# Kernel tuning notes

Measured on AMD Instinct MI355X. Metric: run time of the kernel, lower is better.

Reference implementation:

```python
import jax, jax.numpy as jnp
import numpy as np

D = 640
I = 640
K = 4  # experts per token
E = 32
T = 64
EPS = 1e-5
LIMIT = 7.0


def setup_inputs() -> dict:
    key = jax.random.key(0)
    ks = jax.random.split(key, 8)
    return {
        "x": jax.random.normal(ks[0], (1, D, 1, T), dtype=jnp.float32),
        "norm_w": jax.random.uniform(ks[1], (D,), dtype=jnp.float32) + 0.5,
        "gate_w": jax.random.normal(ks[2], (E, D), dtype=jnp.float32) * 0.05,
        "gate_b": jax.random.normal(ks[3], (E,), dtype=jnp.float32) * 0.05,
        "w1": jax.random.normal(ks[4], (E, D, 2 * I), dtype=jnp.float32) * 0.02,
        "b1": jax.random.normal(ks[5], (E, 2 * I), dtype=jnp.float32) * 0.02,
        "w2": jax.random.normal(ks[6], (E, I, D), dtype=jnp.float32) * 0.02,
        "b2": jax.random.normal(ks[7], (E, D), dtype=jnp.float32) * 0.02,
    }


def reference(x, norm_w, gate_w, gate_b, w1, b1, w2, b2):
    residual = x
    # RMSNorm over channel dim (axis=1) of (1, D, 1, T)
    var = jnp.mean(x * x, axis=1, keepdims=True)
    normed = x * jax.lax.rsqrt(var + EPS) * norm_w.reshape(-1, 1, 1)
    # (1, D, 1, T) -> (T, D)
    t = normed[0, :, 0, :].T
    # router
    g = t @ gate_w.T + gate_b                       # (T, E)
    top_vals, top_idx = jax.lax.top_k(g, K)        # (T, K)
    ew = jax.nn.softmax(top_vals, axis=-1)          # (T, K)
    # gather per-token expert weights (faithful to index_select pattern)
    w1s = w1[top_idx]                               # (T, K, D, 2I)
    b1s = b1[top_idx]                               # (T, K, 2I)
    h = jnp.einsum('td,tkdi->tki', t, w1s) + b1s    # (T, K, 2I)
    h_glu = jnp.minimum(h[..., :I], LIMIT)
    h_lin = jnp.clip(h[..., I:], -LIMIT, LIMIT)
    h_act = h_glu * jax.nn.sigmoid(1.702 * h_glu) * (h_lin + 1.0)  # (T, K, I)
    out = jnp.einsum('tki,tkid->tkd', h_act, w2[top_idx]) + b2[top_idx]  # (T, K, D)
    out = jnp.sum(out * ew[..., None], axis=1)      # (T, D)
    out = out.T[None, :, None, :]                   # (1, D, 1, T)
    return residual + out
```

## Files before the change

### kernel.cpp

```cpp
#include <hip/hip_runtime.h>
#include <math.h>

#define DDIM 640
#define IDIM 640
#define TWO_I 1280
#define KSEL 4
#define NEXP 32
#define NTOK 64
#define NPAIR 256
#define EPSV 1e-5f
#define LIMIT 7.0f
#define CHUNK 8
#define RC 8
#define RLEN 80


__global__ void k_rmsnorm(const float* __restrict__ x, const float* __restrict__ nw,
                          float* __restrict__ tws, int* __restrict__ counts) {
    const int t = blockIdx.x;
    const int tid = threadIdx.x;
    if (blockIdx.x == 0 && tid < NEXP) counts[tid] = 0;
    __shared__ float red[256];
    float s = 0.f;
    for (int d = tid; d < DDIM; d += 256) {
        float v = x[d * NTOK + t];
        s += v * v;
    }
    red[tid] = s;
    __syncthreads();
    for (int off = 128; off > 0; off >>= 1) {
        if (tid < off) red[tid] += red[tid + off];
        __syncthreads();
    }
    const float rs = 1.0f / sqrtf(red[0] * (1.0f / DDIM) + EPSV);
    for (int d = tid; d < DDIM; d += 256) {
        tws[t * DDIM + d] = x[d * NTOK + t] * rs * nw[d];
    }
}

__global__ void k_router(const float* __restrict__ tws, const float* __restrict__ gw,
                         const float* __restrict__ gb, float* __restrict__ ew,
                         int* __restrict__ counts, int* __restrict__ list,
                         int* __restrict__ pexp) {
    const int t = blockIdx.x;
    const int lane = threadIdx.x;
    __shared__ float lg[NEXP];
    if (lane < NEXP) {
        const float* g = gw + lane * DDIM;
        const float* tr = tws + t * DDIM;
        float acc = 0.f;
        for (int d = 0; d < DDIM; d += 4) {
            acc = fmaf(tr[d], g[d], acc);
            acc = fmaf(tr[d + 1], g[d + 1], acc);
            acc = fmaf(tr[d + 2], g[d + 2], acc);
            acc = fmaf(tr[d + 3], g[d + 3], acc);
        }
        lg[lane] = acc + gb[lane];
    }
    __syncthreads();
    if (lane == 0) {
        float vals[KSEL];
        int idx[KSEL];
        for (int k = 0; k < KSEL; ++k) {
            float best = -1e30f;
            int bi = 0;
            for (int e = 0; e < NEXP; ++e) {
                float v = lg[e];
                if (v > best) { best = v; bi = e; }
            }
            vals[k] = best;
            idx[k] = bi;
            lg[bi] = -1e30f;
        }
        const float m = vals[0];
        float ex[KSEL];
        float se = 0.f;
        for (int k = 0; k < KSEL; ++k) { ex[k] = __expf(vals[k] - m); se += ex[k]; }
        const float inv = 1.0f / se;
        for (int k = 0; k < KSEL; ++k) {
            const int p = t * KSEL + k;
            ew[p] = ex[k] * inv;
            pexp[p] = idx[k];
            const int slot = atomicAdd(&counts[idx[k]], 1);
            list[idx[k] * NTOK + slot] = p;
        }
    }
}

__global__ __launch_bounds__(64) void k_ffn1(const float* __restrict__ tws,
                                             const float* __restrict__ w1,
                                             float* __restrict__ hpart,
                                             const int* __restrict__ counts,
                                             const int* __restrict__ list) {
    const int e = blockIdx.y;
    const int rc = blockIdx.z >> 3;
    const int tc = blockIdx.z & 7;
    const int cnt = counts[e];
    const int c0 = tc * CHUNK;
    if (c0 >= cnt) return;
    const int col0 = blockIdx.x * 256 + threadIdx.x * 4;
    const int d0 = rc * RLEN;

    __shared__ float tl[CHUNK][RLEN];
    int pid[CHUNK];
#pragma unroll
    for (int s = 0; s < CHUNK; ++s) {
        int ii = c0 + s;
        ii = (ii < cnt) ? ii : c0;
        pid[s] = list[e * NTOK + ii];
    }
    for (int s = 0; s < CHUNK; ++s) {
        const int tok = pid[s] >> 2;
        for (int d = threadIdx.x; d < RLEN; d += 64)
            tl[s][d] = tws[tok * DDIM + d0 + d];
    }
    __syncthreads();

    const float* wp = w1 + (size_t)e * DDIM * TWO_I + (size_t)d0 * TWO_I + col0;
    float acc[CHUNK][4];
#pragma unroll
    for (int s = 0; s < CHUNK; ++s)
#pragma unroll
        for (int c = 0; c < 4; ++c) acc[s][c] = 0.f;

    for (int dd = 0; dd < RLEN; dd += 8) {
        float4 w[8];
#pragma unroll
        for (int u = 0; u < 8; ++u)
            w[u] = *reinterpret_cast<const float4*>(wp + (size_t)(dd + u) * TWO_I);
#pragma unroll
        for (int u = 0; u < 8; ++u) {
#pragma unroll
            for (int s = 0; s < CHUNK; ++s) {
                const float tv = tl[s][dd + u];
                acc[s][0] = fmaf(tv, w[u].x, acc[s][0]);
                acc[s][1] = fmaf(tv, w[u].y, acc[s][1]);
                acc[s][2] = fmaf(tv, w[u].z, acc[s][2]);
                acc[s][3] = fmaf(tv, w[u].w, acc[s][3]);
            }
        }
    }

#pragma unroll
    for (int s = 0; s < CHUNK; ++s) {
        float4 v = make_float4(acc[s][0], acc[s][1], acc[s][2], acc[s][3]);
        *reinterpret_cast<float4*>(&hpart[((size_t)rc * NPAIR + pid[s]) * TWO_I + col0]) = v;
    }
}

__global__ void k_reduce1(const float* __restrict__ hpart, const float* __restrict__ b1,
                          const int* __restrict__ pexp, float* __restrict__ hact) {
    const int p = blockIdx.x;
    const int e = pexp[p];
    for (int i = threadIdx.x; i < IDIM; i += 256) {
        float g = 0.f, l = 0.f;
#pragma unroll
        for (int rc = 0; rc < RC; ++rc) {
            g += hpart[((size_t)rc * NPAIR + p) * TWO_I + i];
            l += hpart[((size_t)rc * NPAIR + p) * TWO_I + i + IDIM];
        }
        float hg = fminf(g + b1[e * TWO_I + i], LIMIT);
        float hl = l + b1[e * TWO_I + IDIM + i];
        hl = fminf(fmaxf(hl, -LIMIT), LIMIT);
        const float sig = 1.0f / (1.0f + __expf(-1.702f * hg));
        hact[(size_t)p * IDIM + i] = hg * sig * (hl + 1.0f);
    }
}

__global__ __launch_bounds__(64) void k_ffn2(const float* __restrict__ hact,
                                             const float* __restrict__ w2,
                                             float* __restrict__ hpart2,
                                             const int* __restrict__ counts,
                                             const int* __restrict__ list) {
    const int e = blockIdx.y;
    const int rc = blockIdx.z >> 3;
    const int tc = blockIdx.z & 7;
    const int cnt = counts[e];
    const int c0 = tc * CHUNK;
    if (c0 >= cnt) return;
    const int col0 = blockIdx.x * 128 + threadIdx.x * 2;
    const int i0 = rc * RLEN;

    __shared__ float hl[CHUNK][RLEN];
    int pid[CHUNK];
#pragma unroll
    for (int s = 0; s < CHUNK; ++s) {
        int ii = c0 + s;
        ii = (ii < cnt) ? ii : c0;
        pid[s] = list[e * NTOK + ii];
    }
    for (int s = 0; s < CHUNK; ++s) {
        for (int i = threadIdx.x; i < RLEN; i += 64)
            hl[s][i] = hact[(size_t)pid[s] * IDIM + i0 + i];
    }
    __syncthreads();

    const float* wp = w2 + (size_t)e * IDIM * DDIM + (size_t)i0 * DDIM + col0;
    float acc[CHUNK][2];
#pragma unroll
    for (int s = 0; s < CHUNK; ++s) {
        acc[s][0] = 0.f;
        acc[s][1] = 0.f;
    }

    for (int ii = 0; ii < RLEN; ii += 8) {
        float2 w[8];
#pragma unroll
        for (int u = 0; u < 8; ++u)
            w[u] = *reinterpret_cast<const float2*>(wp + (size_t)(ii + u) * DDIM);
#pragma unroll
        for (int u = 0; u < 8; ++u) {
#pragma unroll
            for (int s = 0; s < CHUNK; ++s) {
                const float hv = hl[s][ii + u];
                acc[s][0] = fmaf(hv, w[u].x, acc[s][0]);
                acc[s][1] = fmaf(hv, w[u].y, acc[s][1]);
            }
        }
    }

#pragma unroll
    for (int s = 0; s < CHUNK; ++s) {
        float2 v = make_float2(acc[s][0], acc[s][1]);
        *reinterpret_cast<float2*>(&hpart2[((size_t)rc * NPAIR + pid[s]) * DDIM + col0]) = v;
    }
}

__global__ void k_final(const float* __restrict__ x, const float* __restrict__ hpart2,
                        const float* __restrict__ b2, const float* __restrict__ ew,
                        const int* __restrict__ pexp, float* __restrict__ out) {
    const int t = blockIdx.x;
    for (int d = threadIdx.x; d < DDIM; d += 256) {
        float v = x[d * NTOK + t];
#pragma unroll
        for (int k = 0; k < KSEL; ++k) {
            const int p = t * KSEL + k;
            const int e = pexp[p];
            float s = 0.f;
#pragma unroll
            for (int rc = 0; rc < RC; ++rc)
                s += hpart2[((size_t)rc * NPAIR + p) * DDIM + d];
            v += (s + b2[e * DDIM + d]) * ew[p];
        }
        out[d * NTOK + t] = v;
    }
}

extern "C" void kernel_launch(void* const* d_in, const int* in_sizes, int n_in,
                              void* d_out, int out_size, void* d_ws, size_t ws_size,
                              hipStream_t stream) {
    const float* x  = (const float*)d_in[0];
    const float* nw = (const float*)d_in[1];
    const float* gw = (const float*)d_in[2];
    const float* gb = (const float*)d_in[3];
    const float* w1 = (const float*)d_in[4];
    const float* b1 = (const float*)d_in[5];
    const float* w2 = (const float*)d_in[6];
    const float* b2 = (const float*)d_in[7];
    float* out = (float*)d_out;

    float* ws    = (float*)d_ws;
    float* tws   = ws;
    float* hact  = ws + 40960;
    float* hpart = ws + 204800;
    float* ew    = ws + 2826240;
    int* counts  = (int*)(ws + 2826496);
    int* list    = (int*)(ws + 2826528);
    int* pexp    = (int*)(ws + 2828576);

    hipLaunchKernelGGL(k_rmsnorm, dim3(NTOK), dim3(256), 0, stream, x, nw, tws, counts);
    hipLaunchKernelGGL(k_router, dim3(NTOK), dim3(64), 0, stream, tws, gw, gb, ew, counts, list, pexp);
    hipLaunchKernelGGL(k_ffn1, dim3(5, NEXP, RC * 8), dim3(64), 0, stream, tws, w1, hpart, counts, list);
    hipLaunchKernelGGL(k_reduce1, dim3(NPAIR), dim3(256), 0, stream, hpart, b1, pexp, hact);
    hipLaunchKernelGGL(k_ffn2, dim3(5, NEXP, RC * 8), dim3(64), 0, stream, hact, w2, hpart, counts, list);
    hipLaunchKernelGGL(k_final, dim3(NTOK), dim3(256), 0, stream, x, hpart, b2, ew, pexp, out);
}
```

Baseline: 80.70 us.

## Restructure MoE FFN grids: wider blocks, smaller token chunks, XCD-aware block mapping

Both expert GEMM kernels now run one 320-thread block that covers the full output width instead of five 64-thread blocks. Token chunks shrink from 8 to 4, with 16 chunk slots per expert. The reduction dimension is split into 16 pieces when the workspace is large enough, and a flat block index is remapped so consecutive logical blocks spread across the 8 XCDs. The aim is more parallelism and better load balance for a small, skewed token count. The costs are that each weight row is re-read by more token chunks, and the larger split increases partial-sum traffic through the reduce and final kernels.

```diff
diff --git a/kernel.cpp b/kernel.cpp
--- a/kernel.cpp
+++ b/kernel.cpp
@@ -10,9 +10,9 @@
 #define NPAIR 256
 #define EPSV 1e-5f
 #define LIMIT 7.0f
-#define CHUNK 8
-#define RC 8
-#define RLEN 80
+#define CHUNK 4
+#define NTC 16
+#define MAXRLEN 80
 
 
 __global__ void k_rmsnorm(const float* __restrict__ x, const float* __restrict__ nw,
@@ -87,21 +87,30 @@
     }
 }
 
-__global__ __launch_bounds__(64) void k_ffn1(const float* __restrict__ tws,
-                                             const float* __restrict__ w1,
-                                             float* __restrict__ hpart,
-                                             const int* __restrict__ counts,
-                                             const int* __restrict__ list) {
-    const int e = blockIdx.y;
-    const int rc = blockIdx.z >> 3;
-    const int tc = blockIdx.z & 7;
+__global__ __launch_bounds__(320) void k_ffn1(const float* __restrict__ tws,
+                                              const float* __restrict__ w1,
+                                              float* __restrict__ hpart,
+                                              const int* __restrict__ counts,
+                                              const int* __restrict__ list,
+                                              int nrcMask, int eShift, int rlen) {
+    const int cpx = (int)gridDim.x >> 3;
+    const int L = (blockIdx.x & 7) * cpx + (blockIdx.x >> 3);
+    const int tc = L & (NTC - 1);
+    const int tmp = L >> 4;
+    const int rc = tmp & nrcMask;
+    const int e = tmp >> eShift;
+
     const int cnt = counts[e];
     const int c0 = tc * CHUNK;
     if (c0 >= cnt) return;
-    const int col0 = blockIdx.x * 256 + threadIdx.x * 4;
-    const int d0 = rc * RLEN;
-
-    __shared__ float tl[CHUNK][RLEN];
+    const int tid = threadIdx.x;
+    const int wid = tid >> 6;
+    const int lane = tid & 63;
+    const int col0 = wid * 256 + lane * 4;
+    const int d0 = rc * rlen;
+
+    __shared__ float tl[CHUNK][MAXRLEN];
+
     int pid[CHUNK];
 #pragma unroll
     for (int s = 0; s < CHUNK; ++s) {
@@ -109,30 +118,30 @@
         ii = (ii < cnt) ? ii : c0;
         pid[s] = list[e * NTOK + ii];
     }
-    for (int s = 0; s < CHUNK; ++s) {
-        const int tok = pid[s] >> 2;
-        for (int d = threadIdx.x; d < RLEN; d += 64)
-            tl[s][d] = tws[tok * DDIM + d0 + d];
-    }
+#pragma unroll
+    for (int s = 0; s < CHUNK; ++s)
+        for (int d = tid; d < rlen; d += 320)
+            tl[s][d] = tws[(pid[s] >> 2) * DDIM + d0 + d];
     __syncthreads();
 
     const float* wp = w1 + (size_t)e * DDIM * TWO_I + (size_t)d0 * TWO_I + col0;
+
     float acc[CHUNK][4];
 #pragma unroll
     for (int s = 0; s < CHUNK; ++s)
 #pragma unroll
         for (int c = 0; c < 4; ++c) acc[s][c] = 0.f;
 
-    for (int dd = 0; dd < RLEN; dd += 8) {
+    for (int rb = 0; rb < rlen; rb += 8) {
         float4 w[8];
 #pragma unroll
         for (int u = 0; u < 8; ++u)
-            w[u] = *reinterpret_cast<const float4*>(wp + (size_t)(dd + u) * TWO_I);
+            w[u] = *reinterpret_cast<const float4*>(wp + (size_t)(rb + u) * TWO_I);
 #pragma unroll
         for (int u = 0; u < 8; ++u) {
 #pragma unroll
             for (int s = 0; s < CHUNK; ++s) {
-                const float tv = tl[s][dd + u];
+                const float tv = tl[s][rb + u];
                 acc[s][0] = fmaf(tv, w[u].x, acc[s][0]);
                 acc[s][1] = fmaf(tv, w[u].y, acc[s][1]);
                 acc[s][2] = fmaf(tv, w[u].z, acc[s][2]);
@@ -149,13 +158,12 @@
 }
 
 __global__ void k_reduce1(const float* __restrict__ hpart, const float* __restrict__ b1,
-                          const int* __restrict__ pexp, float* __restrict__ hact) {
+                          const int* __restrict__ pexp, float* __restrict__ hact, int nrc) {
     const int p = blockIdx.x;
     const int e = pexp[p];
     for (int i = threadIdx.x; i < IDIM; i += 256) {
         float g = 0.f, l = 0.f;
-#pragma unroll
-        for (int rc = 0; rc < RC; ++rc) {
+        for (int rc = 0; rc < nrc; ++rc) {
             g += hpart[((size_t)rc * NPAIR + p) * TWO_I + i];
             l += hpart[((size_t)rc * NPAIR + p) * TWO_I + i + IDIM];
         }
@@ -167,21 +175,28 @@
     }
 }
 
-__global__ __launch_bounds__(64) void k_ffn2(const float* __restrict__ hact,
-                                             const float* __restrict__ w2,
-                                             float* __restrict__ hpart2,
-                                             const int* __restrict__ counts,
-                                             const int* __restrict__ list) {
-    const int e = blockIdx.y;
-    const int rc = blockIdx.z >> 3;
-    const int tc = blockIdx.z & 7;
+__global__ __launch_bounds__(320) void k_ffn2(const float* __restrict__ hact,
+                                              const float* __restrict__ w2,
+                                              float* __restrict__ hpart2,
+                                              const int* __restrict__ counts,
+                                              const int* __restrict__ list,
+                                              int nrcMask, int eShift, int rlen) {
+    const int cpx = (int)gridDim.x >> 3;
+    const int L = (blockIdx.x & 7) * cpx + (blockIdx.x >> 3);
+    const int tc = L & (NTC - 1);
+    const int tmp = L >> 4;
+    const int rc = tmp & nrcMask;
+    const int e = tmp >> eShift;
+
     const int cnt = counts[e];
     const int c0 = tc * CHUNK;
     if (c0 >= cnt) return;
-    const int col0 = blockIdx.x * 128 + threadIdx.x * 2;
-    const int i0 = rc * RLEN;
-
-    __shared__ float hl[CHUNK][RLEN];
+    const int tid = threadIdx.x;
+    const int col0 = tid * 2;
+    const int i0 = rc * rlen;
+
+    __shared__ float tl[CHUNK][MAXRLEN];
+
     int pid[CHUNK];
 #pragma unroll
     for (int s = 0; s < CHUNK; ++s) {
@@ -189,30 +204,28 @@
         ii = (ii < cnt) ? ii : c0;
         pid[s] = list[e * NTOK + ii];
     }
-    for (int s = 0; s < CHUNK; ++s) {
-        for (int i = threadIdx.x; i < RLEN; i += 64)
-            hl[s][i] = hact[(size_t)pid[s] * IDIM + i0 + i];
-    }
+#pragma unroll
+    for (int s = 0; s < CHUNK; ++s)
+        for (int d = tid; d < rlen; d += 320)
+            tl[s][d] = hact[(size_t)pid[s] * IDIM + i0 + d];
     __syncthreads();
 
     const float* wp = w2 + (size_t)e * IDIM * DDIM + (size_t)i0 * DDIM + col0;
+
     float acc[CHUNK][2];
 #pragma unroll
-    for (int s = 0; s < CHUNK; ++s) {
-        acc[s][0] = 0.f;
-        acc[s][1] = 0.f;
-    }
-
-    for (int ii = 0; ii < RLEN; ii += 8) {
+    for (int s = 0; s < CHUNK; ++s) { acc[s][0] = 0.f; acc[s][1] = 0.f; }
+
+    for (int rb = 0; rb < rlen; rb += 8) {
         float2 w[8];
 #pragma unroll
         for (int u = 0; u < 8; ++u)
-            w[u] = *reinterpret_cast<const float2*>(wp + (size_t)(ii + u) * DDIM);
+            w[u] = *reinterpret_cast<const float2*>(wp + (size_t)(rb + u) * DDIM);
 #pragma unroll
         for (int u = 0; u < 8; ++u) {
 #pragma unroll
             for (int s = 0; s < CHUNK; ++s) {
-                const float hv = hl[s][ii + u];
+                const float hv = tl[s][rb + u];
                 acc[s][0] = fmaf(hv, w[u].x, acc[s][0]);
                 acc[s][1] = fmaf(hv, w[u].y, acc[s][1]);
             }
@@ -228,7 +241,7 @@
 
 __global__ void k_final(const float* __restrict__ x, const float* __restrict__ hpart2,
                         const float* __restrict__ b2, const float* __restrict__ ew,
-                        const int* __restrict__ pexp, float* __restrict__ out) {
+                        const int* __restrict__ pexp, float* __restrict__ out, int nrc) {
     const int t = blockIdx.x;
     for (int d = threadIdx.x; d < DDIM; d += 256) {
         float v = x[d * NTOK + t];
@@ -237,8 +250,7 @@
             const int p = t * KSEL + k;
             const int e = pexp[p];
             float s = 0.f;
-#pragma unroll
-            for (int rc = 0; rc < RC; ++rc)
+            for (int rc = 0; rc < nrc; ++rc)
                 s += hpart2[((size_t)rc * NPAIR + p) * DDIM + d];
             v += (s + b2[e * DDIM + d]) * ew[p];
         }
@@ -262,16 +274,24 @@
     float* ws    = (float*)d_ws;
     float* tws   = ws;
     float* hact  = ws + 40960;
-    float* hpart = ws + 204800;
-    float* ew    = ws + 2826240;
-    int* counts  = (int*)(ws + 2826496);
-    int* list    = (int*)(ws + 2826528);
-    int* pexp    = (int*)(ws + 2828576);
+    float* ew    = ws + 204800;
+    int* counts  = (int*)(ws + 205056);
+    int* list    = (int*)(ws + 205088);
+    int* pexp    = (int*)(ws + 207136);
+    float* hpart = ws + 207616;
+
+    const size_t need16 = ((size_t)207616 + (size_t)16 * 327680) * 4;
+    const int nrc = (ws_size >= need16) ? 16 : 8;
+    const int eShift = (nrc == 16) ? 4 : 3;
+    const int rlen = DDIM / nrc;
+    const int nblk = NEXP * nrc * NTC;
 
     hipLaunchKernelGGL(k_rmsnorm, dim3(NTOK), dim3(256), 0, stream, x, nw, tws, counts);
     hipLaunchKernelGGL(k_router, dim3(NTOK), dim3(64), 0, stream, tws, gw, gb, ew, counts, list, pexp);
-    hipLaunchKernelGGL(k_ffn1, dim3(5, NEXP, RC * 8), dim3(64), 0, stream, tws, w1, hpart, counts, list);
-    hipLaunchKernelGGL(k_reduce1, dim3(NPAIR), dim3(256), 0, stream, hpart, b1, pexp, hact);
-    hipLaunchKernelGGL(k_ffn2, dim3(5, NEXP, RC * 8), dim3(64), 0, stream, hact, w2, hpart, counts, list);
-    hipLaunchKernelGGL(k_final, dim3(NTOK), dim3(256), 0, stream, x, hpart, b2, ew, pexp, out);
-}
+    hipLaunchKernelGGL(k_ffn1, dim3(nblk), dim3(320), 0, stream, tws, w1, hpart, counts, list,
+                       nrc - 1, eShift, rlen);
+    hipLaunchKernelGGL(k_reduce1, dim3(NPAIR), dim3(256), 0, stream, hpart, b1, pexp, hact, nrc);
+    hipLaunchKernelGGL(k_ffn2, dim3(nblk), dim3(320), 0, stream, hact, w2, hpart, counts, list,
+                       nrc - 1, eShift, rlen);
+    hipLaunchKernelGGL(k_final, dim3(NTOK), dim3(256), 0, stream, x, hpart, b2, ew, pexp, out, nrc);
+}
```

After: 138.5 us. +71.7%, slower.

## Stage expert weight panels into LDS with async double-buffered global_load_lds

Applied to the files above, without the earlier changes.

Both expert FFN kernels become 320-thread blocks (five waves) that each cover the full output width. Weight rows are streamed into a double-buffered LDS panel with global_load_lds, and the next panel's loads overlap the FMAs on the current one. This replaces direct per-thread register loads of weights and is meant to hide memory latency and cut redundant block setup. The cost is about 80 KB of LDS per block, which limits occupancy to one block per CU, plus fewer blocks and reliance on hand-placed vmcnt waits and barriers.

```diff
diff --git a/kernel.cpp b/kernel.cpp
--- a/kernel.cpp
+++ b/kernel.cpp
@@ -13,6 +13,13 @@
 #define CHUNK 8
 #define RC 8
 #define RLEN 80
+
+#define WAITVM(n) asm volatile("s_waitcnt vmcnt(" #n ")" ::: "memory")
+#define RAWBAR() __builtin_amdgcn_s_barrier()
+#define GLL(gp, lp)                                                            \
+    __builtin_amdgcn_global_load_lds(                                          \
+        (const __attribute__((address_space(1))) void*)(gp),                   \
+        (__attribute__((address_space(3))) void*)(lp), 16, 0, 0)
 
 
 __global__ void k_rmsnorm(const float* __restrict__ x, const float* __restrict__ nw,
@@ -87,21 +94,26 @@
     }
 }
 
-__global__ __launch_bounds__(64) void k_ffn1(const float* __restrict__ tws,
-                                             const float* __restrict__ w1,
-                                             float* __restrict__ hpart,
-                                             const int* __restrict__ counts,
-                                             const int* __restrict__ list) {
-    const int e = blockIdx.y;
-    const int rc = blockIdx.z >> 3;
-    const int tc = blockIdx.z & 7;
+__global__ __launch_bounds__(320, 1) void k_ffn1(const float* __restrict__ tws,
+                                                 const float* __restrict__ w1,
+                                                 float* __restrict__ hpart,
+                                                 const int* __restrict__ counts,
+                                                 const int* __restrict__ list) {
+    const int e = blockIdx.x;
+    const int rc = blockIdx.y >> 3;
+    const int tc = blockIdx.y & 7;
     const int cnt = counts[e];
     const int c0 = tc * CHUNK;
     if (c0 >= cnt) return;
-    const int col0 = blockIdx.x * 256 + threadIdx.x * 4;
+    const int tid = threadIdx.x;
+    const int wid = tid >> 6;
+    const int lane = tid & 63;
+    const int col0 = wid * 256 + lane * 4;
     const int d0 = rc * RLEN;
 
+    __shared__ float wlds[2][8 * TWO_I];
     __shared__ float tl[CHUNK][RLEN];
+
     int pid[CHUNK];
 #pragma unroll
     for (int s = 0; s < CHUNK; ++s) {
@@ -109,36 +121,51 @@
         ii = (ii < cnt) ? ii : c0;
         pid[s] = list[e * NTOK + ii];
     }
-    for (int s = 0; s < CHUNK; ++s) {
-        const int tok = pid[s] >> 2;
-        for (int d = threadIdx.x; d < RLEN; d += 64)
-            tl[s][d] = tws[tok * DDIM + d0 + d];
-    }
+#pragma unroll
+    for (int s = 0; s < CHUNK; ++s)
+        for (int d = tid; d < RLEN; d += 320)
+            tl[s][d] = tws[(pid[s] >> 2) * DDIM + d0 + d];
     __syncthreads();
 
-    const float* wp = w1 + (size_t)e * DDIM * TWO_I + (size_t)d0 * TWO_I + col0;
+    const float* wpanel = w1 + (size_t)e * DDIM * TWO_I + (size_t)d0 * TWO_I;
+
     float acc[CHUNK][4];
 #pragma unroll
     for (int s = 0; s < CHUNK; ++s)
 #pragma unroll
         for (int c = 0; c < 4; ++c) acc[s][c] = 0.f;
 
-    for (int dd = 0; dd < RLEN; dd += 8) {
-        float4 w[8];
-#pragma unroll
-        for (int u = 0; u < 8; ++u)
-            w[u] = *reinterpret_cast<const float4*>(wp + (size_t)(dd + u) * TWO_I);
-#pragma unroll
-        for (int u = 0; u < 8; ++u) {
+#pragma unroll
+    for (int k = 0; k < 8; ++k)
+        GLL(wpanel + wid * 2048 + k * 256 + lane * 4, &wlds[0][wid * 2048 + k * 256]);
+
+    for (int t = 0; t < 10; ++t) {
+        const int cur = t & 1;
+        if (t + 1 < 10) {
+            const int nxt = (t + 1) & 1;
+            const float* gsrc = wpanel + (size_t)(t + 1) * 8 * TWO_I;
+#pragma unroll
+            for (int k = 0; k < 8; ++k)
+                GLL(gsrc + wid * 2048 + k * 256 + lane * 4, &wlds[nxt][wid * 2048 + k * 256]);
+            WAITVM(8);
+        } else {
+            WAITVM(0);
+        }
+        RAWBAR();
+#pragma unroll
+        for (int r = 0; r < 8; ++r) {
+            const float4 w = *reinterpret_cast<const float4*>(&wlds[cur][r * TWO_I + col0]);
+            const int row = t * 8 + r;
 #pragma unroll
             for (int s = 0; s < CHUNK; ++s) {
-                const float tv = tl[s][dd + u];
-                acc[s][0] = fmaf(tv, w[u].x, acc[s][0]);
-                acc[s][1] = fmaf(tv, w[u].y, acc[s][1]);
-                acc[s][2] = fmaf(tv, w[u].z, acc[s][2]);
-                acc[s][3] = fmaf(tv, w[u].w, acc[s][3]);
+                const float tv = tl[s][row];
+                acc[s][0] = fmaf(tv, w.x, acc[s][0]);
+                acc[s][1] = fmaf(tv, w.y, acc[s][1]);
+                acc[s][2] = fmaf(tv, w.z, acc[s][2]);
+                acc[s][3] = fmaf(tv, w.w, acc[s][3]);
             }
         }
+        RAWBAR();
     }
 
 #pragma unroll
@@ -167,21 +194,26 @@
     }
 }
 
-__global__ __launch_bounds__(64) void k_ffn2(const float* __restrict__ hact,
-                                             const float* __restrict__ w2,
-                                             float* __restrict__ hpart2,
-                                             const int* __restrict__ counts,
-                                             const int* __restrict__ list) {
-    const int e = blockIdx.y;
-    const int rc = blockIdx.z >> 3;
-    const int tc = blockIdx.z & 7;
+__global__ __launch_bounds__(320, 1) void k_ffn2(const float* __restrict__ hact,
+                                                 const float* __restrict__ w2,
+                                                 float* __restrict__ hpart2,
+                                                 const int* __restrict__ counts,
+                                                 const int* __restrict__ list) {
+    const int e = blockIdx.x;
+    const int rc = blockIdx.y >> 3;
+    const int tc = blockIdx.y & 7;
     const int cnt = counts[e];
     const int c0 = tc * CHUNK;
     if (c0 >= cnt) return;
-    const int col0 = blockIdx.x * 128 + threadIdx.x * 2;
+    const int tid = threadIdx.x;
+    const int wid = tid >> 6;
+    const int lane = tid & 63;
+    const int col0 = tid * 2;
     const int i0 = rc * RLEN;
 
-    __shared__ float hl[CHUNK][RLEN];
+    __shared__ float wlds[2][16 * DDIM];
+    __shared__ float tl[CHUNK][RLEN];
+
     int pid[CHUNK];
 #pragma unroll
     for (int s = 0; s < CHUNK; ++s) {
@@ -189,34 +221,47 @@
         ii = (ii < cnt) ? ii : c0;
         pid[s] = list[e * NTOK + ii];
     }
-    for (int s = 0; s < CHUNK; ++s) {
-        for (int i = threadIdx.x; i < RLEN; i += 64)
-            hl[s][i] = hact[(size_t)pid[s] * IDIM + i0 + i];
-    }
+#pragma unroll
+    for (int s = 0; s < CHUNK; ++s)
+        for (int d = tid; d < RLEN; d += 320)
+            tl[s][d] = hact[(size_t)pid[s] * IDIM + i0 + d];
     __syncthreads();
 
-    const float* wp = w2 + (size_t)e * IDIM * DDIM + (size_t)i0 * DDIM + col0;
+    const float* wpanel = w2 + (size_t)e * IDIM * DDIM + (size_t)i0 * DDIM;
+
     float acc[CHUNK][2];
 #pragma unroll
-    for (int s = 0; s < CHUNK; ++s) {
-        acc[s][0] = 0.f;
-        acc[s][1] = 0.f;
-    }
-
-    for (int ii = 0; ii < RLEN; ii += 8) {
-        float2 w[8];
-#pragma unroll
-        for (int u = 0; u < 8; ++u)
-            w[u] = *reinterpret_cast<const float2*>(wp + (size_t)(ii + u) * DDIM);
-#pragma unroll
-        for (int u = 0; u < 8; ++u) {
+    for (int s = 0; s < CHUNK; ++s) { acc[s][0] = 0.f; acc[s][1] = 0.f; }
+
+#pragma unroll
+    for (int k = 0; k < 8; ++k)
+        GLL(wpanel + wid * 2048 + k * 256 + lane * 4, &wlds[0][wid * 2048 + k * 256]);
+
+    for (int t = 0; t < 5; ++t) {
+        const int cur = t & 1;
+        if (t + 1 < 5) {
+            const int nxt = (t + 1) & 1;
+            const float* gsrc = wpanel + (size_t)(t + 1) * 16 * DDIM;
+#pragma unroll
+            for (int k = 0; k < 8; ++k)
+                GLL(gsrc + wid * 2048 + k * 256 + lane * 4, &wlds[nxt][wid * 2048 + k * 256]);
+            WAITVM(8);
+        } else {
+            WAITVM(0);
+        }
+        RAWBAR();
+#pragma unroll
+        for (int r = 0; r < 16; ++r) {
+            const float2 w = *reinterpret_cast<const float2*>(&wlds[cur][r * DDIM + col0]);
+            const int row = t * 16 + r;
 #pragma unroll
             for (int s = 0; s < CHUNK; ++s) {
-                const float hv = hl[s][ii + u];
-                acc[s][0] = fmaf(hv, w[u].x, acc[s][0]);
-                acc[s][1] = fmaf(hv, w[u].y, acc[s][1]);
+                const float hv = tl[s][row];
+                acc[s][0] = fmaf(hv, w.x, acc[s][0]);
+                acc[s][1] = fmaf(hv, w.y, acc[s][1]);
             }
         }
+        RAWBAR();
     }
 
 #pragma unroll
@@ -270,8 +315,8 @@
 
     hipLaunchKernelGGL(k_rmsnorm, dim3(NTOK), dim3(256), 0, stream, x, nw, tws, counts);
     hipLaunchKernelGGL(k_router, dim3(NTOK), dim3(64), 0, stream, tws, gw, gb, ew, counts, list, pexp);
-    hipLaunchKernelGGL(k_ffn1, dim3(5, NEXP, RC * 8), dim3(64), 0, stream, tws, w1, hpart, counts, list);
+    hipLaunchKernelGGL(k_ffn1, dim3(NEXP, 64), dim3(320), 0, stream, tws, w1, hpart, counts, list);
     hipLaunchKernelGGL(k_reduce1, dim3(NPAIR), dim3(256), 0, stream, hpart, b1, pexp, hact);
-    hipLaunchKernelGGL(k_ffn2, dim3(5, NEXP, RC * 8), dim3(64), 0, stream, hact, w2, hpart, counts, list);
+    hipLaunchKernelGGL(k_ffn2, dim3(NEXP, 64), dim3(320), 0, stream, hact, w2, hpart, counts, list);
     hipLaunchKernelGGL(k_final, dim3(NTOK), dim3(256), 0, stream, x, hpart, b2, ew, pexp, out);
 }
```

New measurement: 86.03 us. 1.07x slower.
